# Kernel tuning notes

Measured on AMD Instinct MI355X. Metric: run time of the kernel, lower is better.

## Reference

```python
import jax, jax.numpy as jnp
import numpy as np

B, K, N = 64, 4096, 256  # batch, num weight groups, group size (n_k)


def setup_inputs() -> dict:
    key = jax.random.key(0)
    kx, kw = jax.random.split(key)
    x = jax.random.normal(kx, (B, K, N), dtype=jnp.float32)
    # scale weights so per-group dot products are O(1) and tanh is not saturated
    W = jax.random.normal(kw, (K, N), dtype=jnp.float32) / np.sqrt(N).astype(np.float32)
    return {"x": x, "W": W}


def reference(x, W):
    # Per-sample block-diagonal matvec: for each sample b and group k,
    # u2[b, k] = sum_n W[k, n] * x[b, k, n]  (tf.linalg.matvec of [1,n_k] weight with z_k),
    # then vCS = tanh(u2). Original returns a list of per-sample K-vectors; we return the
    # stacked [B, K] array, which is the same values.
    u2 = jnp.einsum("bkn,kn->bk", x, W)
    return jnp.tanh(u2)
```

## Files before the change

kernel.cpp:

```cpp
#include <hip/hip_runtime.h>
#include <math.h>

constexpr int GK = 4096;
constexpr int GN = 256;

__global__ __launch_bounds__(256) void ginn_input_layer(
    const float* __restrict__ x,
    const float* __restrict__ W,
    float* __restrict__ out)
{
    const int lane = threadIdx.x & 63;
    const int wave = threadIdx.x >> 6;
    const long long row = (long long)blockIdx.x * 4 + wave;
    const int k = (int)(row & (GK - 1));

    const float4 xv = ((const float4*)(x + row * GN))[lane];
    const float4 wv = ((const float4*)(W + (long long)k * GN))[lane];

    float s = xv.x * wv.x + xv.y * wv.y + xv.z * wv.z + xv.w * wv.w;

    #pragma unroll
    for (int off = 32; off > 0; off >>= 1)
        s += __shfl_down(s, off, 64);

    if (lane == 0)
        out[row] = tanhf(s);
}

extern "C" void kernel_launch(void* const* d_in, const int* in_sizes, int n_in,
                              void* d_out, int out_size, void* d_ws, size_t ws_size,
                              hipStream_t stream) {
    const float* x = (const float*)d_in[0];
    const float* W = (const float*)d_in[1];
    float* out = (float*)d_out;

    const int rows = out_size;
    const int blocks = rows / 4;
    ginn_input_layer<<<blocks, 256, 0, stream>>>(x, W, out);
}
```

Measured before the change: 343.7 us.

## Process sixteen rows per wave with batched loads and nontemporal x reads

Each wavefront now handles sixteen consecutive rows in groups of four. It issues four x and W vector loads before reducing, interleaves four xor-shuffle reductions, and writes four tanh outputs with one vector store. x is read with nontemporal loads so the streamed input does not pollute the cache. The goal is more memory-level parallelism per wave and less per-row launch and reduction overhead, at the cost of 16x fewer waves in the grid.

```diff
diff --git a/kernel.cpp b/kernel.cpp
--- a/kernel.cpp
+++ b/kernel.cpp
@@ -3,28 +3,51 @@
 
 constexpr int GK = 4096;
 constexpr int GN = 256;
+constexpr int ROWS_PER_WAVE = 16;
+
+typedef float f32x4 __attribute__((ext_vector_type(4)));
 
 __global__ __launch_bounds__(256) void ginn_input_layer(
     const float* __restrict__ x,
     const float* __restrict__ W,
     float* __restrict__ out)
 {
-    const int lane = threadIdx.x & 63;
-    const int wave = threadIdx.x >> 6;
-    const long long row = (long long)blockIdx.x * 4 + wave;
-    const int k = (int)(row & (GK - 1));
+    const int lane   = threadIdx.x & 63;
+    const int waveId = (int)((blockIdx.x * blockDim.x + threadIdx.x) >> 6);
+    const long long row0 = (long long)waveId * ROWS_PER_WAVE;
+    const int k0 = (int)(row0 & (GK - 1));
 
-    const float4 xv = ((const float4*)(x + row * GN))[lane];
-    const float4 wv = ((const float4*)(W + (long long)k * GN))[lane];
-
-    float s = xv.x * wv.x + xv.y * wv.y + xv.z * wv.z + xv.w * wv.w;
+    const f32x4* xp = (const f32x4*)(x + row0 * GN) + lane;
+    const f32x4* wp = (const f32x4*)(W + (long long)k0 * GN) + lane;
 
     #pragma unroll
-    for (int off = 32; off > 0; off >>= 1)
-        s += __shfl_down(s, off, 64);
-
-    if (lane == 0)
-        out[row] = tanhf(s);
+    for (int rb = 0; rb < ROWS_PER_WAVE; rb += 4) {
+        f32x4 xv[4], wv[4];
+        #pragma unroll
+        for (int j = 0; j < 4; ++j) {
+            xv[j] = __builtin_nontemporal_load(xp + (long long)(rb + j) * (GN / 4));
+            wv[j] = wp[(long long)(rb + j) * (GN / 4)];
+        }
+        float s[4];
+        #pragma unroll
+        for (int j = 0; j < 4; ++j) {
+            s[j] = fmaf(xv[j].x, wv[j].x,
+                   fmaf(xv[j].y, wv[j].y,
+                   fmaf(xv[j].z, wv[j].z, xv[j].w * wv[j].w)));
+        }
+        #pragma unroll
+        for (int off = 32; off > 0; off >>= 1) {
+            #pragma unroll
+            for (int j = 0; j < 4; ++j)
+                s[j] += __shfl_xor(s[j], off, 64);
+        }
+        if (lane == 0) {
+            f32x4 o;
+            o.x = tanhf(s[0]); o.y = tanhf(s[1]);
+            o.z = tanhf(s[2]); o.w = tanhf(s[3]);
+            *(f32x4*)(out + row0 + rb) = o;
+        }
+    }
 }
 
 extern "C" void kernel_launch(void* const* d_in, const int* in_sizes, int n_in,
@@ -34,7 +57,6 @@
     const float* W = (const float*)d_in[1];
     float* out = (float*)d_out;
 
-    const int rows = out_size;
-    const int blocks = rows / 4;
+    const int blocks = out_size / (4 * ROWS_PER_WAVE);
     ginn_input_layer<<<blocks, 256, 0, stream>>>(x, W, out);
 }
```

Measured after the change: 337.9 us, median of 2. Within noise of the previous version (-1.7%).
